# Kernel optimization log

Measured on AMD Instinct MI355X. Metric: run time of the kernel, lower is better.

The kernel has to match this reference:

```python
import jax, jax.numpy as jnp
import numpy as np
import math

B, L, D, H = 4, 2048, 1024, 16
HD = D // H  # head dim = 64


def setup_inputs() -> dict:
    key = jax.random.key(0)
    ks = jax.random.split(key, 5)
    s = 1.0 / math.sqrt(D)
    return {
        "x": jax.random.normal(ks[0], (B, L, D), dtype=jnp.float32),
        "Wqkv": jax.random.normal(ks[1], (D, 3 * D), dtype=jnp.float32) * s,
        "bqkv": jax.random.normal(ks[2], (3 * D,), dtype=jnp.float32) * 0.02,
        "Wproj": jax.random.normal(ks[3], (D, D), dtype=jnp.float32) * s,
        "bproj": jax.random.normal(ks[4], (D,), dtype=jnp.float32) * 0.02,
    }


def reference(x, Wqkv, bqkv, Wproj, bproj):
    Bsz, Ls, Ds = x.shape
    qkv = x @ Wqkv + bqkv                     # [B, L, 3D]
    q, k, v = jnp.split(qkv, 3, axis=-1)      # each [B, L, D]

    def heads(t):  # [B, L, D] -> [B, H, L, HD]
        return t.reshape(Bsz, Ls, H, HD).transpose(0, 2, 1, 3)

    q, k, v = heads(q), heads(k), heads(v)
    att = jnp.einsum("bhqd,bhkd->bhqk", q, k) / jnp.sqrt(jnp.float32(HD))
    causal = jnp.tril(jnp.ones((Ls, Ls), dtype=bool))
    att = jnp.where(causal[None, None], att, -jnp.inf)
    att = jax.nn.softmax(att, axis=-1)
    y = jnp.einsum("bhqk,bhkd->bhqd", att, v)  # [B, H, L, HD]
    y = y.transpose(0, 2, 1, 3).reshape(Bsz, Ls, Ds)
    return y @ Wproj + bproj
```

## Files before the change

kernel.cpp:

```cpp
#include <hip/hip_runtime.h>


typedef __bf16 bf16x2 __attribute__((ext_vector_type(2)));
typedef __bf16 bf16x4 __attribute__((ext_vector_type(4)));
typedef __bf16 bf16x8 __attribute__((ext_vector_type(8)));
typedef float f32x4 __attribute__((ext_vector_type(4)));
typedef float f32x16 __attribute__((ext_vector_type(16)));
typedef unsigned u32x4 __attribute__((ext_vector_type(4)));

#define MFMA16(a, b, c) __builtin_amdgcn_mfma_f32_16x16x32_bf16(a, b, c, 0, 0, 0)
#define MFMA32(a, b, c) __builtin_amdgcn_mfma_f32_32x32x16_bf16(a, b, c, 0, 0, 0)

__device__ __forceinline__ void gload_lds16(const __bf16* g, __bf16* l) {
    __builtin_amdgcn_global_load_lds(
        (const __attribute__((address_space(1))) void*)g,
        (__attribute__((address_space(3))) void*)l, 16, 0, 0);
}

__device__ __forceinline__ unsigned pkbf(float a, float b) {
    bf16x2 t = {(__bf16)a, (__bf16)b};
    return __builtin_bit_cast(unsigned, t);
}

__global__ void fused_convert_kernel(const float* __restrict__ x, __bf16* __restrict__ xb,
                                     const float* __restrict__ wqkv, __bf16* __restrict__ wqkvT,
                                     const float* __restrict__ wproj, __bf16* __restrict__ wprojT)
{
    const int blk = blockIdx.x;
    if (blk < 4096) {
        int i = (blk * 256 + threadIdx.x) * 8;
        f32x4 lo = *(const f32x4*)&x[i];
        f32x4 hi = *(const f32x4*)&x[i + 4];
        bf16x8 o;
#pragma unroll
        for (int j = 0; j < 4; ++j) { o[j] = (__bf16)lo[j]; o[j + 4] = (__bf16)hi[j]; }
        *(bf16x8*)&xb[i] = o;
        return;
    }
    __shared__ __bf16 t[32][33];
    const float* in;
    __bf16* out;
    int R, C, bx, by;
    if (blk < 7168) {
        int b2 = blk - 4096;
        bx = b2 % 96; by = b2 / 96; in = wqkv; out = wqkvT; R = 1024; C = 3072;
    } else {
        int b2 = blk - 7168;
        bx = b2 % 32; by = b2 / 32; in = wproj; out = wprojT; R = 1024; C = 1024;
    }
    const int c0 = bx * 32, r0 = by * 32;
    const int tx = threadIdx.x & 31, ty = threadIdx.x >> 5;
#pragma unroll
    for (int j = 0; j < 4; ++j) {
        int r = ty + j * 8;
        t[tx][r] = (__bf16)in[(size_t)(r0 + r) * C + c0 + tx];
    }
    __syncthreads();
#pragma unroll
    for (int j = 0; j < 4; ++j) {
        int r = ty + j * 8;
        out[(size_t)(c0 + r) * R + r0 + tx] = t[r][tx];
    }
}

#define GEMM_TILE_LOOP(Abase, Bbase)                                               \
    for (int k0 = 0; k0 < 1024; k0 += 64) {                                        \
        __syncthreads();                                                           \
        _Pragma("unroll")                                                          \
        for (int l = 0; l < 4; ++l) {                                              \
            int base = l * 256 + w * 64;                                           \
            int r = (base >> 3) + (lane >> 3);                                     \
            int c = (lane & 7) ^ (r & 7);                                          \
            gload_lds16(&Abase[(size_t)(m0 + r) * 1024 + k0 + c * 8], &As[base * 8]); \
            gload_lds16(&Bbase[(size_t)(n0 + r) * 1024 + k0 + c * 8], &Bs[base * 8]); \
        }                                                                          \
        __syncthreads();                                                           \
        bf16x8 af[2][4], bfr[2][4];                                                \
        _Pragma("unroll")                                                          \
        for (int kk = 0; kk < 2; ++kk) {                                           \
            _Pragma("unroll")                                                      \
            for (int mf = 0; mf < 4; ++mf) {                                       \
                int rr = wr * 64 + mf * 16 + row;                                  \
                af[kk][mf] = *(const bf16x8*)                                      \
                    &As[rr * 64 + (((kk * 4 + g) ^ (rr & 7)) * 8)];                \
            }                                                                      \
            _Pragma("unroll")                                                      \
            for (int nf = 0; nf < 4; ++nf) {                                       \
                int rr = wc * 64 + nf * 16 + row;                                  \
                bfr[kk][nf] = *(const bf16x8*)                                     \
                    &Bs[rr * 64 + (((kk * 4 + g) ^ (rr & 7)) * 8)];                \
            }                                                                      \
        }                                                                          \
        _Pragma("unroll")                                                          \
        for (int kk = 0; kk < 2; ++kk)                                             \
            _Pragma("unroll")                                                      \
            for (int mf = 0; mf < 4; ++mf)                                         \
                _Pragma("unroll")                                                  \
                for (int nf = 0; nf < 4; ++nf)                                     \
                    acc[mf][nf] = MFMA16(af[kk][mf], bfr[kk][nf], acc[mf][nf]);    \
    }

__global__ __launch_bounds__(256, 2)
void qkv_gemm_kernel(const __bf16* __restrict__ A, const __bf16* __restrict__ Bt,
                     const float* __restrict__ bias,
                     __bf16* __restrict__ q2, __bf16* __restrict__ k2,
                     __bf16* __restrict__ v2)
{
    __shared__ __bf16 stage[16384];
    __bf16* const As = stage;
    __bf16* const Bs = stage + 8192;
    const int tid = threadIdx.x;
    const int lane = tid & 63;
    const int w = tid >> 6;
    const int wr = w >> 1, wc = w & 1;
    const int row = lane & 15, g = lane >> 4;
    const int m0 = blockIdx.x * 128;
    const int n0 = blockIdx.y * 128;

    const f32x4 fzero = {0.f, 0.f, 0.f, 0.f};
    f32x4 acc[4][4];
#pragma unroll
    for (int a = 0; a < 4; ++a)
#pragma unroll
        for (int b = 0; b < 4; ++b) acc[a][b] = fzero;

    GEMM_TILE_LOOP(A, Bt)

    __syncthreads();
    const int part = n0 >> 10;
    const float QSCL = 0.18033688f;
    if (part == 2) {
#pragma unroll
        for (int mf = 0; mf < 4; ++mf)
#pragma unroll
            for (int nf = 0; nf < 4; ++nf) {
                int nl = nf * 16 + row;
                float bv = bias[n0 + wc * 64 + nl];
                bf16x4 pv;
#pragma unroll
                for (int i = 0; i < 4; ++i)
                    pv[i] = (__bf16)(acc[mf][nf][i] + bv);
                int c = (mf >> 1) * 4 + (nl >> 5) * 2 + (mf & 1);
                int off0 = (g & 1) * 256 + (nl & 31) * 8 + ((g >> 1) & 1) * 4;
                *(unsigned long long*)&stage[w * 4096 + c * 512 + off0] =
                    __builtin_bit_cast(unsigned long long, pv);
            }
    } else {
#pragma unroll
        for (int mf = 0; mf < 4; ++mf)
#pragma unroll
            for (int nf = 0; nf < 4; ++nf) {
                int nl = nf * 16 + row;
                float bv = bias[n0 + wc * 64 + nl];
#pragma unroll
                for (int i = 0; i < 4; ++i) {
                    int ml = mf * 16 + g * 4 + i;
                    float fv = acc[mf][nf][i] + bv;
                    if (part == 0) fv *= QSCL;
                    int c = (ml >> 5) * 4 + (nl >> 4);
                    int off = ((nl >> 3) & 1) * 256 + (ml & 31) * 8 + (nl & 7);
                    stage[w * 4096 + c * 512 + off] = (__bf16)fv;
                }
            }
    }
    {
        const int b = m0 >> 11;
        const int lbase5 = (m0 & 2047) >> 5;
        const int hh = ((n0 & 1023) >> 6) + wc;
        const size_t bh64 = (size_t)(b * 16 + hh) * 64;
        __bf16* dst = part == 0 ? q2 : (part == 1 ? k2 : v2);
#pragma unroll
        for (int c = 0; c < 8; ++c) {
            bf16x8 val = *(const bf16x8*)&stage[w * 4096 + c * 512 + lane * 8];
            size_t gbase = ((bh64 + lbase5 + wr * 2 + (c >> 2)) * 4 + (c & 3)) * 512;
            *(bf16x8*)&dst[gbase + lane * 8] = val;
        }
    }
}

__global__ __launch_bounds__(256, 2)
void proj_gemm_kernel(const __bf16* __restrict__ A, const __bf16* __restrict__ Bt,
                      const float* __restrict__ bias, float* __restrict__ out)
{
    __shared__ __bf16 As[128 * 64];
    __shared__ __bf16 Bs[128 * 64];
    const int tid = threadIdx.x;
    const int lane = tid & 63;
    const int w = tid >> 6;
    const int wr = w >> 1, wc = w & 1;
    const int row = lane & 15, g = lane >> 4;
    const int m0 = blockIdx.x * 128;
    const int n0 = blockIdx.y * 128;

    const f32x4 fzero = {0.f, 0.f, 0.f, 0.f};
    f32x4 acc[4][4];
#pragma unroll
    for (int a = 0; a < 4; ++a)
#pragma unroll
        for (int b = 0; b < 4; ++b) acc[a][b] = fzero;

    GEMM_TILE_LOOP(A, Bt)

#pragma unroll
    for (int mf = 0; mf < 4; ++mf)
#pragma unroll
        for (int nf = 0; nf < 4; ++nf) {
            int n = n0 + wc * 64 + nf * 16 + row;
            float bv = bias[n];
#pragma unroll
            for (int i = 0; i < 4; ++i) {
                int mm = m0 + wr * 64 + mf * 16 + g * 4 + i;
                out[(size_t)mm * 1024 + n] = acc[mf][nf][i] + bv;
            }
        }
}

__global__ __launch_bounds__(128, 2)
void attn_kernel(const __bf16* __restrict__ Q2, const __bf16* __restrict__ K2,
                 const __bf16* __restrict__ V2, __bf16* __restrict__ Yw)
{
    const int tid = threadIdx.x;
    const int lane = tid & 63;
    const int wv = tid >> 6;
    const int col = lane & 31;
    const int hi = lane >> 5;
    const int i0 = blockIdx.x;
    const int bh = (i0 & 7) * 8 + ((i0 >> 3) & 7);
    const int t = (i0 >> 6) * 2 + wv;
    const int tB = 63 - t;
    const int qA = t * 32;
    const int qB = tB * 32;
    const size_t tb = (size_t)bh * 64;

    bf16x8 qfA[4], qfB[4];
#pragma unroll
    for (int dc = 0; dc < 4; ++dc) {
        qfA[dc] = *(const bf16x8*)&Q2[((tb + t) * 4 + dc) * 512 + lane * 8];
        qfB[dc] = *(const bf16x8*)&Q2[((tb + tB) * 4 + dc) * 512 + lane * 8];
    }

    bf16x8 ones;
#pragma unroll
    for (int j = 0; j < 8; ++j) ones[j] = (__bf16)1.0f;

    f32x16 CZ;
#pragma unroll
    for (int i = 0; i < 16; ++i) CZ[i] = 0.f;

    f32x16 OtA[2], OtB[2], OsA, OsB;
#pragma unroll
    for (int dt = 0; dt < 2; ++dt)
#pragma unroll
        for (int i = 0; i < 16; ++i) { OtA[dt][i] = 0.f; OtB[dt][i] = 0.f; }
#pragma unroll
    for (int i = 0; i < 16; ++i) { OsA[i] = 0.f; OsB[i] = 0.f; }

    auto smxpack = [&](f32x16& st, f32x16& Os, bool diag,
                       bf16x8& pa0, bf16x8& pa1) {
        if (diag) {
#pragma unroll
            for (int r = 0; r < 16; ++r) {
                int crow = (r & 3) + 8 * (r >> 2) + 4 * hi;
                if (crow > col) st[r] = -1e30f;
            }
        }
#pragma unroll
        for (int r = 0; r < 16; ++r) st[r] = exp2f(st[r]);
        u32x4 w0 = {pkbf(st[0], st[1]), pkbf(st[2], st[3]),
                    pkbf(st[4], st[5]), pkbf(st[6], st[7])};
        u32x4 w1 = {pkbf(st[8], st[9]), pkbf(st[10], st[11]),
                    pkbf(st[12], st[13]), pkbf(st[14], st[15])};
        pa0 = __builtin_bit_cast(bf16x8, w0);
        pa1 = __builtin_bit_cast(bf16x8, w1);
        Os = MFMA32(ones, pa0, Os);
        Os = MFMA32(ones, pa1, Os);
    };

    const __bf16* kp = K2 + tb * 2048 + lane * 8;
    const __bf16* vp = V2 + tb * 2048 + lane * 8;

    bf16x8 kfP[4], vfP[4];
#pragma unroll
    for (int dc = 0; dc < 4; ++dc) {
        kfP[dc] = *(const bf16x8*)&kp[dc * 512];
        vfP[dc] = *(const bf16x8*)&vp[dc * 512];
    }

    const int nsteps = tB + 1;
    for (int kt = 0; kt < nsteps; ++kt) {
        const bool dual = (kt <= t);

        f32x16 stA, stB;
        __builtin_amdgcn_s_setprio(1);
        stB = MFMA32(kfP[0], qfB[0], CZ);
        stB = MFMA32(kfP[1], qfB[1], stB);
        stB = MFMA32(kfP[2], qfB[2], stB);
        stB = MFMA32(kfP[3], qfB[3], stB);
        if (dual) {
            stA = MFMA32(kfP[0], qfA[0], CZ);
            stA = MFMA32(kfP[1], qfA[1], stA);
            stA = MFMA32(kfP[2], qfA[2], stA);
            stA = MFMA32(kfP[3], qfA[3], stA);
        }
        __builtin_amdgcn_s_setprio(0);

        kp += 2048;
#pragma unroll
        for (int dc = 0; dc < 4; ++dc)
            kfP[dc] = *(const bf16x8*)&kp[dc * 512];

        bf16x8 paA0, paA1, paB0, paB1;
        smxpack(stB, OsB, kt == tB, paB0, paB1);
        if (dual) smxpack(stA, OsA, kt == t, paA0, paA1);

        __builtin_amdgcn_s_setprio(1);
        OtB[0] = MFMA32(vfP[0], paB0, OtB[0]);
        OtB[0] = MFMA32(vfP[1], paB1, OtB[0]);
        OtB[1] = MFMA32(vfP[2], paB0, OtB[1]);
        OtB[1] = MFMA32(vfP[3], paB1, OtB[1]);
        if (dual) {
            OtA[0] = MFMA32(vfP[0], paA0, OtA[0]);
            OtA[0] = MFMA32(vfP[1], paA1, OtA[0]);
            OtA[1] = MFMA32(vfP[2], paA0, OtA[1]);
            OtA[1] = MFMA32(vfP[3], paA1, OtA[1]);
        }
        __builtin_amdgcn_s_setprio(0);

        vp += 2048;
#pragma unroll
        for (int dc = 0; dc < 4; ++dc)
            vfP[dc] = *(const bf16x8*)&vp[dc * 512];
    }

    const int b = bh >> 4, h = bh & 15;
    const float invA = 1.f / OsA[0], invB = 1.f / OsB[0];
    __bf16* yrowA = Yw + ((size_t)(b * 2048 + qA + col)) * 1024 + h * 64;
    __bf16* yrowB = Yw + ((size_t)(b * 2048 + qB + col)) * 1024 + h * 64;
#pragma unroll
    for (int dt = 0; dt < 2; ++dt)
#pragma unroll
        for (int rg = 0; rg < 4; ++rg) {
            int d0 = dt * 32 + rg * 8 + hi * 4;
            unsigned lo = pkbf(OtA[dt][rg * 4 + 0] * invA, OtA[dt][rg * 4 + 1] * invA);
            unsigned h2 = pkbf(OtA[dt][rg * 4 + 2] * invA, OtA[dt][rg * 4 + 3] * invA);
            *(unsigned long long*)&yrowA[d0] =
                (unsigned long long)lo | ((unsigned long long)h2 << 32);
            lo = pkbf(OtB[dt][rg * 4 + 0] * invB, OtB[dt][rg * 4 + 1] * invB);
            h2 = pkbf(OtB[dt][rg * 4 + 2] * invB, OtB[dt][rg * 4 + 3] * invB);
            *(unsigned long long*)&yrowB[d0] =
                (unsigned long long)lo | ((unsigned long long)h2 << 32);
        }
}

extern "C" void kernel_launch(void* const* d_in, const int* in_sizes, int n_in,
                              void* d_out, int out_size, void* d_ws, size_t ws_size,
                              hipStream_t stream)
{
    const float* x     = (const float*)d_in[0];
    const float* wqkv  = (const float*)d_in[1];
    const float* bqkv  = (const float*)d_in[2];
    const float* wproj = (const float*)d_in[3];
    const float* bproj = (const float*)d_in[4];
    float* out = (float*)d_out;

    const size_t E = (size_t)4 * 16 * 2048 * 64;
    __bf16* q2     = (__bf16*)d_ws;
    __bf16* k2     = q2 + E;
    __bf16* v2     = k2 + E;
    __bf16* xb     = v2 + E;
    __bf16* y      = xb;
    __bf16* wqkvT  = xb + E;
    __bf16* wprojT = wqkvT + (size_t)3072 * 1024;

    fused_convert_kernel<<<8192, 256, 0, stream>>>(x, xb, wqkv, wqkvT, wproj, wprojT);
    qkv_gemm_kernel<<<dim3(64, 24), 256, 0, stream>>>(xb, wqkvT, bqkv, q2, k2, v2);
    attn_kernel<<<1024, 128, 0, stream>>>(q2, k2, v2, y);
    proj_gemm_kernel<<<dim3(64, 8), 256, 0, stream>>>(y, wprojT, bproj, out);
}
```

Before: 151.9 us.

## Double-buffer LDS tiles in QKV and projection GEMMs to overlap loads with MFMA

Splits the GEMM main loop into stage and compute macros and alternates between two LDS buffers, so global-to-LDS loads for the next K tile are issued while MFMAs run on the current tile. It also raises wave priority around the MFMA block with s_setprio. This removes the load-then-wait bubble of each K step at the cost of doubling LDS per block to 64 KB, which may limit occupancy to two blocks per CU (matching launch_bounds). It also relies on the async global_load_lds completing before the following barrier.

Measured after the change: 151.4 us. About the same (-0.3%).

```diff
diff --git a/kernel.cpp b/kernel.cpp
--- a/kernel.cpp
+++ b/kernel.cpp
@@ -63,18 +63,18 @@
     }
 }
 
-#define GEMM_TILE_LOOP(Abase, Bbase)                                               \
-    for (int k0 = 0; k0 < 1024; k0 += 64) {                                        \
-        __syncthreads();                                                           \
-        _Pragma("unroll")                                                          \
-        for (int l = 0; l < 4; ++l) {                                              \
-            int base = l * 256 + w * 64;                                           \
-            int r = (base >> 3) + (lane >> 3);                                     \
-            int c = (lane & 7) ^ (r & 7);                                          \
-            gload_lds16(&Abase[(size_t)(m0 + r) * 1024 + k0 + c * 8], &As[base * 8]); \
-            gload_lds16(&Bbase[(size_t)(n0 + r) * 1024 + k0 + c * 8], &Bs[base * 8]); \
-        }                                                                          \
-        __syncthreads();                                                           \
+#define GEMM_STAGE(Abase, Bbase, Adst, Bdst, k0s)                                  \
+    _Pragma("unroll")                                                              \
+    for (int l = 0; l < 4; ++l) {                                                  \
+        int base = l * 256 + w * 64;                                               \
+        int r = (base >> 3) + (lane >> 3);                                         \
+        int c = (lane & 7) ^ (r & 7);                                              \
+        gload_lds16(&Abase[(size_t)(m0 + r) * 1024 + (k0s) + c * 8], &Adst[base * 8]); \
+        gload_lds16(&Bbase[(size_t)(n0 + r) * 1024 + (k0s) + c * 8], &Bdst[base * 8]); \
+    }
+
+#define GEMM_COMPUTE(Asrc, Bsrc)                                                   \
+    {                                                                              \
         bf16x8 af[2][4], bfr[2][4];                                                \
         _Pragma("unroll")                                                          \
         for (int kk = 0; kk < 2; ++kk) {                                           \
@@ -82,15 +82,16 @@
             for (int mf = 0; mf < 4; ++mf) {                                       \
                 int rr = wr * 64 + mf * 16 + row;                                  \
                 af[kk][mf] = *(const bf16x8*)                                      \
-                    &As[rr * 64 + (((kk * 4 + g) ^ (rr & 7)) * 8)];                \
+                    &Asrc[rr * 64 + (((kk * 4 + g) ^ (rr & 7)) * 8)];              \
             }                                                                      \
             _Pragma("unroll")                                                      \
             for (int nf = 0; nf < 4; ++nf) {                                       \
                 int rr = wc * 64 + nf * 16 + row;                                  \
                 bfr[kk][nf] = *(const bf16x8*)                                     \
-                    &Bs[rr * 64 + (((kk * 4 + g) ^ (rr & 7)) * 8)];                \
+                    &Bsrc[rr * 64 + (((kk * 4 + g) ^ (rr & 7)) * 8)];              \
             }                                                                      \
         }                                                                          \
+        __builtin_amdgcn_s_setprio(1);                                             \
         _Pragma("unroll")                                                          \
         for (int kk = 0; kk < 2; ++kk)                                             \
             _Pragma("unroll")                                                      \
@@ -98,6 +99,21 @@
                 _Pragma("unroll")                                                  \
                 for (int nf = 0; nf < 4; ++nf)                                     \
                     acc[mf][nf] = MFMA16(af[kk][mf], bfr[kk][nf], acc[mf][nf]);    \
+        __builtin_amdgcn_s_setprio(0);                                             \
+    }
+
+#define GEMM_TILE_LOOP(Abase, Bbase)                                               \
+    GEMM_STAGE(Abase, Bbase, As0, Bs0, 0)                                          \
+    __syncthreads();                                                               \
+    for (int k2 = 0; k2 < 1024; k2 += 128) {                                       \
+        GEMM_STAGE(Abase, Bbase, As1, Bs1, k2 + 64)                                \
+        GEMM_COMPUTE(As0, Bs0)                                                     \
+        __syncthreads();                                                           \
+        if (k2 + 128 < 1024) {                                                     \
+            GEMM_STAGE(Abase, Bbase, As0, Bs0, k2 + 128)                           \
+        }                                                                          \
+        GEMM_COMPUTE(As1, Bs1)                                                     \
+        __syncthreads();                                                           \
     }
 
 __global__ __launch_bounds__(256, 2)
@@ -106,9 +122,11 @@
                      __bf16* __restrict__ q2, __bf16* __restrict__ k2,
                      __bf16* __restrict__ v2)
 {
-    __shared__ __bf16 stage[16384];
-    __bf16* const As = stage;
-    __bf16* const Bs = stage + 8192;
+    __shared__ __bf16 stage[32768];
+    __bf16* const As0 = stage;
+    __bf16* const Bs0 = stage + 8192;
+    __bf16* const As1 = stage + 16384;
+    __bf16* const Bs1 = stage + 24576;
     const int tid = threadIdx.x;
     const int lane = tid & 63;
     const int w = tid >> 6;
@@ -126,7 +144,6 @@
 
     GEMM_TILE_LOOP(A, Bt)
 
-    __syncthreads();
     const int part = n0 >> 10;
     const float QSCL = 0.18033688f;
     if (part == 2) {
@@ -182,8 +199,11 @@
 void proj_gemm_kernel(const __bf16* __restrict__ A, const __bf16* __restrict__ Bt,
                       const float* __restrict__ bias, float* __restrict__ out)
 {
-    __shared__ __bf16 As[128 * 64];
-    __shared__ __bf16 Bs[128 * 64];
+    __shared__ __bf16 stage[32768];
+    __bf16* const As0 = stage;
+    __bf16* const Bs0 = stage + 8192;
+    __bf16* const As1 = stage + 16384;
+    __bf16* const Bs1 = stage + 24576;
     const int tid = threadIdx.x;
     const int lane = tid & 63;
     const int w = tid >> 6;
```
